# Kernel tuning notes

Measured on AMD Instinct MI355X. Metric: run time of the kernel, lower is better.

The kernel has to match this reference:

```python
import jax, jax.numpy as jnp
import numpy as np

N = 50000       # nodes
E = 800000      # edges
IN = 256        # input channels
H = 4           # heads
C = 64          # hidden channels per head
NEG_SLOPE = 0.2 # PyG GATConv default LeakyReLU slope
EPS = 1e-16


def setup_inputs() -> dict:
    key = jax.random.key(0)
    k_x, k_e, k_w, k_as, k_ad = jax.random.split(key, 5)
    x = jax.random.normal(k_x, (N, IN), dtype=jnp.float32)
    edge_index = jax.random.randint(k_e, (2, E), 0, N, dtype=jnp.int64)
    # GATConv params: glorot-style scale
    W = jax.random.normal(k_w, (IN, H * C), dtype=jnp.float32) * (1.0 / np.sqrt(IN))
    att_src = jax.random.normal(k_as, (H, C), dtype=jnp.float32) * (1.0 / np.sqrt(C))
    att_dst = jax.random.normal(k_ad, (H, C), dtype=jnp.float32) * (1.0 / np.sqrt(C))
    return {"x": x, "edge_index": edge_index, "W": W, "att_src": att_src, "att_dst": att_dst}


def reference(x, edge_index, W, att_src, att_dst):
    src, dst = edge_index[0], edge_index[1]
    # linear projection, split heads: [N, H, C]
    xh = (x @ W).reshape(N, H, C)
    # per-node attention halves: [N, H]
    a_src = jnp.einsum('nhc,hc->nh', xh, att_src)
    a_dst = jnp.einsum('nhc,hc->nh', xh, att_dst)
    # per-edge logits with LeakyReLU: [E, H]
    alpha = a_src[src] + a_dst[dst]
    alpha = jnp.where(alpha >= 0, alpha, NEG_SLOPE * alpha)
    # segment softmax over destination nodes
    m = jax.ops.segment_max(alpha, dst, num_segments=N)          # [N, H]
    ex = jnp.exp(alpha - m[dst])                                  # [E, H]
    denom = jax.ops.segment_sum(ex, dst, num_segments=N)         # [N, H]
    att = ex / (denom[dst] + EPS)                                 # [E, H]
    # weighted message scatter-add: [N, H, C] -> concat heads [N, H*C]
    msg = att[:, :, None] * xh[src]                               # [E, H, C]
    out = jax.ops.segment_sum(msg, dst, num_segments=N)
    out = out.reshape(N, H * C)
    return (out, att)
```

## Files before the change

### kernel.cpp

```cpp
#include <hip/hip_runtime.h>
#include <math.h>

#define IN_CH   256
#define HC      256
#define H_HEADS 4
#define NEG_SLOPE 0.2f
#define LOG2E   1.44269504088896f
#define MINIT   -3.0e38f

typedef __attribute__((ext_vector_type(8))) short short8;
typedef __attribute__((ext_vector_type(4))) float float4v;
typedef __attribute__((ext_vector_type(2))) unsigned uint2v;

__device__ __forceinline__ float bf2f(unsigned short b) {
    return __uint_as_float(((unsigned)b) << 16);
}
__device__ __forceinline__ float blo(unsigned u) {
    return __uint_as_float(u << 16);
}
__device__ __forceinline__ float bhi(unsigned u) {
    return __uint_as_float(u & 0xffff0000u);
}
__device__ __forceinline__ unsigned short f2bf(float f) {
    unsigned u = __float_as_uint(f);
    u += 0x7fffu + ((u >> 16) & 1u);
    return (unsigned short)(u >> 16);
}
__device__ __forceinline__ float lrelu(float a) {
    return a >= 0.f ? a : NEG_SLOPE * a;
}
__device__ __forceinline__ float fexp2(float a) {
    return __builtin_amdgcn_exp2f(a);
}


__global__ void prep_w(const float* __restrict__ w,
                       unsigned short* __restrict__ wt) {
    int idx = blockIdx.x * 256 + threadIdx.x;
    int k = idx >> 8, c = idx & 255;
    wt[(size_t)c * 256 + k] = f2bf(w[idx]);
}

__global__ __launch_bounds__(256) void gemm_xh(const float* __restrict__ x,
                                               const unsigned short* __restrict__ wt,
                                               const float* __restrict__ att_s,
                                               const float* __restrict__ att_d,
                                               unsigned short* __restrict__ xh_pl,
                                               float* __restrict__ a_src,
                                               float* __restrict__ a_dst, int N) {
    __shared__ __attribute__((aligned(16))) unsigned char lds_a[16384];
    int tid  = threadIdx.x;
    int wave = tid >> 6;
    int lane = tid & 63;
    int quad = lane >> 4;
    int l16  = lane & 15;
    int rb   = blockIdx.x * 16;

#pragma unroll
    for (int pass = 0; pass < 2; ++pass) {
        int s  = pass * 256 + tid;
        int kc = s >> 4;
        int m  = s & 15;
        int grow = rb + m; if (grow >= N) grow = N - 1;
        const float* gp = x + (size_t)grow * IN_CH + kc * 8;
        float4v f0 = *(const float4v*)gp;
        float4v f1 = *(const float4v*)(gp + 4);
        short8 hi, lo;
#pragma unroll
        for (int j = 0; j < 4; ++j) {
            unsigned short h0 = f2bf(f0[j]);
            hi[j] = (short)h0;
            lo[j] = (short)f2bf(f0[j] - bf2f(h0));
            unsigned short h1 = f2bf(f1[j]);
            hi[4 + j] = (short)h1;
            lo[4 + j] = (short)f2bf(f1[j] - bf2f(h1));
        }
        *(short8*)(lds_a + (size_t)s * 16) = hi;
        *(short8*)(lds_a + 8192 + (size_t)s * 16) = lo;
    }
    __syncthreads();

    float4v acc[4] = {};
    const unsigned short* wt_base = wt + ((size_t)wave * 64 + l16) * IN_CH;
#pragma unroll
    for (int k0 = 0; k0 < 8; ++k0) {
        int kc   = k0 * 4 + quad;
        int slot = kc * 16 + l16;
        short8 a_hi = *(const short8*)(lds_a + slot * 16);
        short8 a_lo = *(const short8*)(lds_a + 8192 + slot * 16);
#pragma unroll
        for (int ct = 0; ct < 4; ++ct) {
            short8 bh = *(const short8*)(wt_base + (size_t)ct * 16 * IN_CH
                                         + k0 * 32 + quad * 8);
            acc[ct] = __builtin_amdgcn_mfma_f32_16x16x32_bf16(a_lo, bh, acc[ct], 0, 0, 0);
            acc[ct] = __builtin_amdgcn_mfma_f32_16x16x32_bf16(a_hi, bh, acc[ct], 0, 0, 0);
        }
    }

    int cb = wave;
    float ps[4] = {0.f, 0.f, 0.f, 0.f};
    float pd[4] = {0.f, 0.f, 0.f, 0.f};
#pragma unroll
    for (int ct = 0; ct < 4; ++ct) {
        float as_c = att_s[cb * 64 + ct * 16 + l16] * LOG2E;
        float ad_c = att_d[cb * 64 + ct * 16 + l16] * LOG2E;
        int ch = cb * 64 + ct * 16 + l16;
        int pl = ch >> 5, wc = ch & 31;
#pragma unroll
        for (int r = 0; r < 4; ++r) {
            float v = acc[ct][r];
            int grow = rb + quad * 4 + r;
            if (grow < N)
                xh_pl[((size_t)pl * N + grow) * 32 + wc] = f2bf(v);
            ps[r] += v * as_c;
            pd[r] += v * ad_c;
        }
    }
#pragma unroll
    for (int off = 1; off < 16; off <<= 1) {
#pragma unroll
        for (int r = 0; r < 4; ++r) {
            ps[r] += __shfl_xor(ps[r], off);
            pd[r] += __shfl_xor(pd[r], off);
        }
    }
    if (l16 == 0) {
#pragma unroll
        for (int r = 0; r < 4; ++r) {
            int grow = rb + quad * 4 + r;
            if (grow < N) {
                a_src[(size_t)grow * 4 + cb] = ps[r];
                a_dst[(size_t)grow * 4 + cb] = pd[r];
            }
        }
    }
}

__global__ __launch_bounds__(256) void deg_count(const int* __restrict__ ei,
                                                 int* __restrict__ deg, int E) {
    int e = blockIdx.x * 256 + threadIdx.x;
    if (e >= E) return;
    atomicAdd(deg + ei[E + e], 1);
}

__global__ __launch_bounds__(256) void scan_part(const int* __restrict__ deg,
                                                 int* __restrict__ part, int N) {
    int t = threadIdx.x;
    int base = blockIdx.x * 1024 + t * 4;
    int s = 0;
    if (base + 4 <= N) {
        int4 v = *(const int4*)(deg + base);
        s = v.x + v.y + v.z + v.w;
    } else {
#pragma unroll
        for (int j = 0; j < 4; ++j)
            if (base + j < N) s += deg[base + j];
    }
#pragma unroll
    for (int off = 1; off < 64; off <<= 1) s += __shfl_xor(s, off);
    __shared__ int ws[4];
    if ((t & 63) == 0) ws[t >> 6] = s;
    __syncthreads();
    if (t == 0) part[blockIdx.x] = ws[0] + ws[1] + ws[2] + ws[3];
}

__global__ __launch_bounds__(256) void scan_final(const int* __restrict__ deg,
                                                  const int* __restrict__ part,
                                                  int* __restrict__ rowptr,
                                                  int* __restrict__ cursor, int N) {
    __shared__ int sm[256];
    __shared__ int wsum[4];
    int t = threadIdx.x;
    int bacc = 0;
    for (int j = t; j < blockIdx.x; j += 256) bacc += part[j];
#pragma unroll
    for (int off = 1; off < 64; off <<= 1) bacc += __shfl_xor(bacc, off);
    if ((t & 63) == 0) wsum[t >> 6] = bacc;

    int base = blockIdx.x * 1024 + t * 4;
    int v0 = 0, v1 = 0, v2 = 0, v3 = 0;
    if (base + 4 <= N) {
        int4 v = *(const int4*)(deg + base);
        v0 = v.x; v1 = v.y; v2 = v.z; v3 = v.w;
    } else {
        if (base + 0 < N) v0 = deg[base + 0];
        if (base + 1 < N) v1 = deg[base + 1];
        if (base + 2 < N) v2 = deg[base + 2];
        if (base + 3 < N) v3 = deg[base + 3];
    }
    int s = v0 + v1 + v2 + v3;
    sm[t] = s;
    __syncthreads();
    for (int off = 1; off < 256; off <<= 1) {
        int tmp = (t >= off) ? sm[t - off] : 0;
        __syncthreads();
        sm[t] += tmp;
        __syncthreads();
    }
    int boff = wsum[0] + wsum[1] + wsum[2] + wsum[3];
    int run = boff + sm[t] - s;
    int r0 = run, r1 = r0 + v0, r2 = r1 + v1, r3 = r2 + v2;
    if (base + 4 <= N) {
        *(int4*)(rowptr + base) = (int4){r0, r1, r2, r3};
        *(int4*)(cursor + base) = (int4){r0, r1, r2, r3};
    } else {
        if (base + 0 < N) { rowptr[base + 0] = r0; cursor[base + 0] = r0; }
        if (base + 1 < N) { rowptr[base + 1] = r1; cursor[base + 1] = r1; }
        if (base + 2 < N) { rowptr[base + 2] = r2; cursor[base + 2] = r2; }
        if (base + 3 < N) { rowptr[base + 3] = r3; cursor[base + 3] = r3; }
    }
}

__global__ __launch_bounds__(256) void fill_csr(const int* __restrict__ ei,
                                                int* __restrict__ cursor,
                                                int* __restrict__ csr_off6, int E) {
    int e = blockIdx.x * 256 + threadIdx.x;
    if (e >= E) return;
    int s = ei[e], d = ei[E + e];
    int slot = atomicAdd(cursor + d, 1);
    csr_off6[slot] = s << 6;
}

__global__ __launch_bounds__(256) void softmax_stats(const int* __restrict__ csr_off6,
                                                     const float* __restrict__ a_src,
                                                     const float* __restrict__ a_dst,
                                                     const int* __restrict__ rowptr,
                                                     const int* __restrict__ deg,
                                                     float* __restrict__ pack,
                                                     float* __restrict__ p_soa,
                                                     int N, int E) {
    int d = blockIdx.x * 256 + threadIdx.x;
    int h = blockIdx.y;
    if (d >= N) return;
    int start = rowptr[d], cnt = deg[d];
    float adh = a_dst[(size_t)d * 4 + h];
    const int* offs = csr_off6 + start;
    float m = MINIT, l = 0.f;
    for (int i = 0; i < cnt; ++i) {
        int off = offs[i];
        float al = lrelu(a_src[(off >> 4) + h] + adh);
        float mn = fmaxf(m, al);
        l = l * fexp2(m - mn) + fexp2(al - mn);
        m = mn;
    }
    float inv = 1.f / (l + 1e-16f);
    pack[(size_t)d * 8 + h]     = m;
    pack[(size_t)d * 8 + 4 + h] = inv;
    float* pout = p_soa + (size_t)h * E + start;
    for (int i = 0; i < cnt; ++i) {
        int off = offs[i];
        float al = lrelu(a_src[(off >> 4) + h] + adh);
        pout[i] = fexp2(al - m) * inv;
    }
}

__global__ __launch_bounds__(256) void gat_planes(const int* __restrict__ csr_off6,
                                                  const float* __restrict__ p_soa,
                                                  const int* __restrict__ rowptr,
                                                  const int* __restrict__ deg,
                                                  const unsigned short* __restrict__ xh_pl,
                                                  float* __restrict__ out, int N, int E) {
    int tid = threadIdx.x;
    int g   = blockIdx.x & 7;
    int db  = blockIdx.x >> 3;
    int grp = tid >> 3;
    int l8  = tid & 7;
    int d   = db * 32 + grp;
    bool dv = d < N;
    int dc  = dv ? d : N - 1;
    int start = rowptr[dc];
    int cnt   = dv ? deg[dc] : 0;
    int h = g >> 1;

    int cw = cnt;
    cw = max(cw, __shfl_xor(cw, 8));
    cw = max(cw, __shfl_xor(cw, 16));
    cw = max(cw, __shfl_xor(cw, 32));

    const char* pb = (const char*)xh_pl + (size_t)g * N * 64;
    const float* ph = p_soa + (size_t)h * E + start;
    int lb = l8 * 8;

    float a0 = 0.f, a1 = 0.f, a2 = 0.f, a3 = 0.f;

#define POFF(i) (((i) < cnt) ? csr_off6[start + (i)] : 0)
#define PPV(i)  (((i) < cnt) ? ph[i] : 0.f)

    int   oE  = POFF(0), oO  = POFF(1);
    float pE  = PPV(0),  pO  = PPV(1);
    int   oE1 = POFF(2), oO1 = POFF(3);
    float pE1 = PPV(2),  pO1 = PPV(3);

#pragma unroll 2
    for (int i = 0; i < cw; i += 2) {
        uint2v xE = *(const uint2v*)(pb + (size_t)(unsigned)oE + lb);
        uint2v xO = *(const uint2v*)(pb + (size_t)(unsigned)oO + lb);
        int   oE2 = POFF(i + 4), oO2 = POFF(i + 5);
        float pE2 = PPV(i + 4),  pO2 = PPV(i + 5);

        a0 += pE * blo(xE[0]); a1 += pE * bhi(xE[0]);
        a2 += pE * blo(xE[1]); a3 += pE * bhi(xE[1]);
        a0 += pO * blo(xO[0]); a1 += pO * bhi(xO[0]);
        a2 += pO * blo(xO[1]); a3 += pO * bhi(xO[1]);

        oE = oE1; oO = oO1; oE1 = oE2; oO1 = oO2;
        pE = pE1; pO = pO1; pE1 = pE2; pO1 = pO2;
    }
#undef POFF
#undef PPV

    if (dv) {
        float4v o;
        o[0] = a0; o[1] = a1; o[2] = a2; o[3] = a3;
        *(float4v*)(out + (size_t)d * HC + g * 32 + l8 * 4) = o;
    }
}

__global__ __launch_bounds__(256) void att_edge(const int* __restrict__ ei,
                                                const float* __restrict__ a_src,
                                                const float* __restrict__ a_dst,
                                                const float* __restrict__ pack,
                                                float* __restrict__ att_out, int E) {
    int e = blockIdx.x * 256 + threadIdx.x;
    if (e >= E) return;
    int s = ei[e], d = ei[E + e];
    float4v as = *(const float4v*)(a_src + (size_t)s * 4);
    float4v ad = *(const float4v*)(a_dst + (size_t)d * 4);
    float4v mm = *(const float4v*)(pack + (size_t)d * 8);
    float4v gg = *(const float4v*)(pack + (size_t)d * 8 + 4);
    float4v o;
#pragma unroll
    for (int h = 0; h < 4; ++h)
        o[h] = fexp2(lrelu(as[h] + ad[h]) - mm[h]) * gg[h];
    *(float4v*)(att_out + (size_t)e * 4) = o;
}

extern "C" void kernel_launch(void* const* d_in, const int* in_sizes, int n_in,
                              void* d_out, int out_size, void* d_ws, size_t ws_size,
                              hipStream_t stream) {
    const float* x     = (const float*)d_in[0];
    const int*   ei    = (const int*)d_in[1];
    const float* W     = (const float*)d_in[2];
    const float* att_s = (const float*)d_in[3];
    const float* att_d = (const float*)d_in[4];

    const int N = in_sizes[0] / IN_CH;
    const int E = in_sizes[1] / 2;

    char* ws = (char*)d_ws;
    size_t off = 0;
    unsigned short* xh_pl = (unsigned short*)(ws + off); off += (size_t)N * HC * 2;
    unsigned short* wt    = (unsigned short*)(ws + off); off += (size_t)IN_CH * HC * 2;
    float* a_src = (float*)(ws + off); off += (size_t)N * H_HEADS * 4;
    float* a_dst = (float*)(ws + off); off += (size_t)N * H_HEADS * 4;
    float* pack  = (float*)(ws + off); off += (size_t)N * 8 * 4;
    int* rowptr  = (int*)(ws + off); off += (size_t)N * 4;
    int* cursor  = (int*)(ws + off); off += (size_t)N * 4;
    int* csr_off6 = (int*)(ws + off); off += (size_t)E * 4;
    float* p_soa = (float*)(ws + off); off += (size_t)E * 4 * 4;
    int* part    = (int*)(ws + off); off += 1024 * 4;
    size_t zoff = off;
    int* deg     = (int*)(ws + off); off += (size_t)N * 4;

    float* out     = (float*)d_out;
    float* out_att = out + (size_t)N * HC;

    (void)hipMemsetAsync(ws + zoff, 0, off - zoff, stream);

    const int NB  = (N + 1023) / 1024;
    const int NDB = (N + 31) / 32;

    prep_w<<<256, 256, 0, stream>>>(W, wt);
    deg_count<<<(E + 255) / 256, 256, 0, stream>>>(ei, deg, E);
    gemm_xh<<<(N + 15) / 16, 256, 0, stream>>>(x, wt, att_s, att_d,
                                               xh_pl, a_src, a_dst, N);
    scan_part<<<NB, 256, 0, stream>>>(deg, part, N);
    scan_final<<<NB, 256, 0, stream>>>(deg, part, rowptr, cursor, N);
    fill_csr<<<(E + 255) / 256, 256, 0, stream>>>(ei, cursor, csr_off6, E);
    softmax_stats<<<dim3((N + 255) / 256, 4), 256, 0, stream>>>(csr_off6, a_src, a_dst,
                                                                rowptr, deg, pack,
                                                                p_soa, N, E);
    gat_planes<<<NDB * 8, 256, 0, stream>>>(csr_off6, p_soa, rowptr, deg,
                                            xh_pl, out, N, E);
    att_edge<<<(E + 255) / 256, 256, 0, stream>>>(ei, a_src, a_dst, pack,
                                                  out_att, E);
}
```

Before: 391.5 us.

## Parallelize softmax_stats with 16 lanes per (node, head) using shuffle reductions

softmax_stats previously used one thread per (destination node, head) and walked its edges serially, so degree skew caused divergence and memory accesses were uncoalesced. Now 16 lanes cooperate on each (node, head), loading 16 edges at a time, combining max and sum through xor-shuffle reductions with an online-softmax update, and writing normalized probabilities in coalesced chunks. With an average degree near 16 most lanes stay busy, at the cost of shuffle overhead and partly idle lanes on low-degree nodes.

```diff
diff --git a/kernel.cpp b/kernel.cpp
--- a/kernel.cpp
+++ b/kernel.cpp
@@ -229,28 +229,46 @@
                                                      float* __restrict__ pack,
                                                      float* __restrict__ p_soa,
                                                      int N, int E) {
-    int d = blockIdx.x * 256 + threadIdx.x;
-    int h = blockIdx.y;
+    int tid = threadIdx.x;
+    int grp = tid >> 4;
+    int l16 = tid & 15;
+    int h   = grp & 3;
+    int d   = blockIdx.x * 4 + (grp >> 2);
     if (d >= N) return;
     int start = rowptr[d], cnt = deg[d];
     float adh = a_dst[(size_t)d * 4 + h];
     const int* offs = csr_off6 + start;
+
     float m = MINIT, l = 0.f;
-    for (int i = 0; i < cnt; ++i) {
-        int off = offs[i];
-        float al = lrelu(a_src[(off >> 4) + h] + adh);
-        float mn = fmaxf(m, al);
-        l = l * fexp2(m - mn) + fexp2(al - mn);
+    for (int base = 0; base < cnt; base += 16) {
+        int idx = base + l16;
+        bool v = idx < cnt;
+        int off = v ? offs[idx] : 0;
+        float al = v ? lrelu(a_src[(off >> 4) + h] + adh) : -INFINITY;
+        float cm = al;
+#pragma unroll
+        for (int j = 1; j < 16; j <<= 1) cm = fmaxf(cm, __shfl_xor(cm, j, 16));
+        float mn = fmaxf(m, cm);
+        float p = fexp2(al - mn);
+        float cs = p;
+#pragma unroll
+        for (int j = 1; j < 16; j <<= 1) cs += __shfl_xor(cs, j, 16);
+        l = l * fexp2(m - mn) + cs;
         m = mn;
     }
     float inv = 1.f / (l + 1e-16f);
-    pack[(size_t)d * 8 + h]     = m;
-    pack[(size_t)d * 8 + 4 + h] = inv;
+    if (l16 == 0) {
+        pack[(size_t)d * 8 + h]     = m;
+        pack[(size_t)d * 8 + 4 + h] = inv;
+    }
     float* pout = p_soa + (size_t)h * E + start;
-    for (int i = 0; i < cnt; ++i) {
-        int off = offs[i];
-        float al = lrelu(a_src[(off >> 4) + h] + adh);
-        pout[i] = fexp2(al - m) * inv;
+    for (int base = 0; base < cnt; base += 16) {
+        int idx = base + l16;
+        if (idx < cnt) {
+            int off = offs[idx];
+            float al = lrelu(a_src[(off >> 4) + h] + adh);
+            pout[idx] = fexp2(al - m) * inv;
+        }
     }
 }
 
@@ -377,9 +395,8 @@
     scan_part<<<NB, 256, 0, stream>>>(deg, part, N);
     scan_final<<<NB, 256, 0, stream>>>(deg, part, rowptr, cursor, N);
     fill_csr<<<(E + 255) / 256, 256, 0, stream>>>(ei, cursor, csr_off6, E);
-    softmax_stats<<<dim3((N + 255) / 256, 4), 256, 0, stream>>>(csr_off6, a_src, a_dst,
-                                                                rowptr, deg, pack,
-                                                                p_soa, N, E);
+    softmax_stats<<<(N + 3) / 4, 256, 0, stream>>>(csr_off6, a_src, a_dst,
+                                                   rowptr, deg, pack, p_soa, N, E);
     gat_planes<<<NDB * 8, 256, 0, stream>>>(csr_off6, p_soa, rowptr, deg,
                                             xh_pl, out, N, E);
     att_edge<<<(E + 255) / 256, 256, 0, stream>>>(ei, a_src, a_dst, pack,
```

Result: faster. 348.5 us (-11.0%).
